# Performance work log

Measured on AMD Instinct MI355X. Metric: run time of the kernel, lower is better.

Reference implementation:

```python
import jax, jax.numpy as jnp
import numpy as np

N_POINTS = 64
N_COLS = 500000
N_ANGS = N_POINTS * (N_POINTS - 1) // 2  # 2016


def setup_inputs() -> dict:
    key = jax.random.key(0)
    k1, k2 = jax.random.split(key)
    X = jax.random.normal(k1, (N_POINTS, N_COLS), dtype=jnp.float32)
    angles = 0.1 * jax.random.normal(k2, (N_ANGS,), dtype=jnp.float32)
    mus = jnp.ones((N_POINTS,), dtype=jnp.float32)
    return {"X": X, "angles": angles, "mus": mus}


def reference(X, angles, mus):
    # X: [n, m]; apply n(n-1)/2 sequential Givens rotations over row pairs
    # in order (iTop, iBtm) for iTop < iBtm, then scale rows by mus.
    # Original torch math per pair: vt' = c*vt - s*vb ; vb' = s*vt + c*vb.
    n = X.shape[0]
    top_np, btm_np = np.triu_indices(n, k=1)  # row-major order matches the double loop
    top = jnp.asarray(top_np, dtype=jnp.int32)
    btm = jnp.asarray(btm_np, dtype=jnp.int32)

    def step(Y, inp):
        a, it, ib = inp
        c = jnp.cos(a)
        s = jnp.sin(a)
        vt = Y[it]  # [m]
        vb = Y[ib]  # [m]
        Y = Y.at[it].set(c * vt - s * vb)
        Y = Y.at[ib].set(s * vt + c * vb)
        return Y, None

    Y, _ = jax.lax.scan(step, X, (angles, top, btm))
    return Y * mus[:, None]
```

## Files before the change

kernel.cpp:

```cpp
#include <hip/hip_runtime.h>
#include <hip/hip_bf16.h>

#define NPTS  64
#define NCOLS 500000
#define NANG  2016

typedef __attribute__((ext_vector_type(8))) short bf16x8;
typedef __attribute__((ext_vector_type(4))) float f32x4;

static __device__ inline short f2bf(float f) {
    union { float f; unsigned u; } uf; uf.f = f;
    unsigned u = uf.u;
    unsigned r = (u + 0x7fffu + ((u >> 16) & 1u)) >> 16;
    return (short)r;
}

__global__ __launch_bounds__(64) void build_M(const float* __restrict__ angles,
                                              const float* __restrict__ mus,
                                              float* __restrict__ Mout) {
    __shared__ float cs[NANG];
    __shared__ float sn[NANG];
    const int tid = threadIdx.x;

    for (int k = tid; k < NANG; k += 64) {
        float a = angles[k];
        cs[k] = cosf(a);
        sn[k] = sinf(a);
    }
    __syncthreads();

    float q[NPTS];
#pragma unroll
    for (int j = 0; j < NPTS; ++j) q[j] = (j == tid) ? 1.0f : 0.0f;

    int k = 0;
#pragma unroll
    for (int i = 0; i < NPTS - 1; ++i) {
#pragma unroll
        for (int ib = i + 1; ib < NPTS; ++ib, ++k) {
            float c = cs[k], s = sn[k];
            float t = q[i];
            float b = q[ib];
            q[ib] = s * t + c * b;
            q[i]  = c * t - s * b;
        }
    }

#pragma unroll
    for (int row = 0; row < NPTS; ++row)
        Mout[row * NPTS + tid] = mus[row] * q[row];
}

__global__ __launch_bounds__(256) void apply_M(const float* __restrict__ X,
                                               const float* __restrict__ M,
                                               float* __restrict__ out,
                                               int nfull, int wstride) {
    const int lane  = threadIdx.x & 63;
    const int wave  = threadIdx.x >> 6;
    const int laneN = lane & 15;
    const int quad  = lane >> 4;

    bf16x8 afrag[4][2];
#pragma unroll
    for (int t = 0; t < 4; ++t) {
#pragma unroll
        for (int q = 0; q < 2; ++q) {
            const float* src = M + (t * 16 + laneN) * NPTS + q * 32 + quad * 8;
            bf16x8 f;
#pragma unroll
            for (int j = 0; j < 8; ++j) f[j] = f2bf(src[j]);
            afrag[t][q] = f;
        }
    }

    const int gw = blockIdx.x * 4 + wave;

    for (int s = gw; s < nfull; s += wstride) {
        const long col0 = (long)s * 64 + 4 * laneN;
        const float* xb = X + col0;

        bf16x8 bfrag[4][2];
#pragma unroll
        for (int q = 0; q < 2; ++q) {
#pragma unroll
            for (int j = 0; j < 8; ++j) {
                const int kk = q * 32 + quad * 8 + j;
                f32x4 v = *(const f32x4*)(xb + (long)kk * NCOLS);
#pragma unroll
                for (int u = 0; u < 4; ++u)
                    bfrag[u][q][j] = f2bf(v[u]);
            }
        }

#pragma unroll
        for (int t = 0; t < 4; ++t) {
            f32x4 acc[4];
#pragma unroll
            for (int u = 0; u < 4; ++u) {
                f32x4 a = {0.f, 0.f, 0.f, 0.f};
                a = __builtin_amdgcn_mfma_f32_16x16x32_bf16(afrag[t][0], bfrag[u][0], a, 0, 0, 0);
                a = __builtin_amdgcn_mfma_f32_16x16x32_bf16(afrag[t][1], bfrag[u][1], a, 0, 0, 0);
                acc[u] = a;
            }
#pragma unroll
            for (int rr = 0; rr < 4; ++rr) {
                const int row = t * 16 + quad * 4 + rr;
                f32x4 o = { acc[0][rr], acc[1][rr], acc[2][rr], acc[3][rr] };
                *(f32x4*)(out + (long)row * NCOLS + col0) = o;
            }
        }
    }

    if (gw < 2) {
        const int col = nfull * 64 + gw * 16 + laneN;
        const float* xb = X + col;
        bf16x8 bfrag[2];
#pragma unroll
        for (int q = 0; q < 2; ++q) {
            bf16x8 f;
#pragma unroll
            for (int j = 0; j < 8; ++j)
                f[j] = f2bf(xb[(long)(q * 32 + quad * 8 + j) * NCOLS]);
            bfrag[q] = f;
        }
#pragma unroll
        for (int t = 0; t < 4; ++t) {
            f32x4 a = {0.f, 0.f, 0.f, 0.f};
            a = __builtin_amdgcn_mfma_f32_16x16x32_bf16(afrag[t][0], bfrag[0], a, 0, 0, 0);
            a = __builtin_amdgcn_mfma_f32_16x16x32_bf16(afrag[t][1], bfrag[1], a, 0, 0, 0);
#pragma unroll
            for (int rr = 0; rr < 4; ++rr)
                out[(long)(t * 16 + quad * 4 + rr) * NCOLS + col] = a[rr];
        }
    }
}

extern "C" void kernel_launch(void* const* d_in, const int* in_sizes, int n_in,
                              void* d_out, int out_size, void* d_ws, size_t ws_size,
                              hipStream_t stream) {
    const float* X      = (const float*)d_in[0];
    const float* angles = (const float*)d_in[1];
    const float* mus    = (const float*)d_in[2];
    float* out = (float*)d_out;
    float* M   = (float*)d_ws;

    build_M<<<1, 64, 0, stream>>>(angles, mus, M);

    const int nfull  = NCOLS / 64;
    const int blocks = 1024;
    apply_M<<<blocks, 256, 0, stream>>>(X, M, out, nfull, blocks * 4);
}
```

Baseline: 322.3 us.

## Parallelize rotation-matrix build into chunk products and combine, use nontemporal stores

The serial single-block build of the 64x64 rotation matrix is split into four blocks, each computing the product of a contiguous chunk of Givens rotations. Two combine launches then multiply the partial products together, applying mus in the last one. The output stores in apply_M become nontemporal, and the grid grows to 1953 blocks so each wave handles about one column tile. The aim is to shorten the serial prologue and improve streaming write behavior, at the cost of two extra small kernel launches.

Measured after the change: 280.6 us. 1.15x faster.

```diff
diff --git a/kernel.cpp b/kernel.cpp
--- a/kernel.cpp
+++ b/kernel.cpp
@@ -15,40 +15,89 @@
     return (short)r;
 }
 
-__global__ __launch_bounds__(64) void build_M(const float* __restrict__ angles,
-                                              const float* __restrict__ mus,
-                                              float* __restrict__ Mout) {
-    __shared__ float cs[NANG];
-    __shared__ float sn[NANG];
+static __host__ __device__ constexpr int rotS(int i) { return 63 * i - i * (i - 1) / 2; }
+
+template<int I0, int I1>
+__device__ __forceinline__ void chunk_body(const float* __restrict__ angles,
+                                           float* __restrict__ P,
+                                           float2* csn) {
+    constexpr int K0 = rotS(I0);
+    constexpr int NK = rotS(I1) - K0;
     const int tid = threadIdx.x;
 
-    for (int k = tid; k < NANG; k += 64) {
-        float a = angles[k];
-        cs[k] = cosf(a);
-        sn[k] = sinf(a);
+    for (int t = tid; t < NK; t += 64) {
+        float s, c;
+        sincosf(angles[K0 + t], &s, &c);
+        csn[t] = make_float2(c, s);
     }
     __syncthreads();
 
-    float q[NPTS];
-#pragma unroll
-    for (int j = 0; j < NPTS; ++j) q[j] = (j == tid) ? 1.0f : 0.0f;
+    float q[64 - I0];
+#pragma unroll
+    for (int r = I0; r < 64; ++r) q[r - I0] = (r == tid) ? 1.0f : 0.0f;
 
     int k = 0;
 #pragma unroll
-    for (int i = 0; i < NPTS - 1; ++i) {
-#pragma unroll
-        for (int ib = i + 1; ib < NPTS; ++ib, ++k) {
-            float c = cs[k], s = sn[k];
-            float t = q[i];
-            float b = q[ib];
-            q[ib] = s * t + c * b;
-            q[i]  = c * t - s * b;
-        }
-    }
-
-#pragma unroll
-    for (int row = 0; row < NPTS; ++row)
-        Mout[row * NPTS + tid] = mus[row] * q[row];
+    for (int i = I0; i < I1; ++i) {
+#pragma unroll
+        for (int ib = i + 1; ib < 64; ++ib, ++k) {
+            float c = csn[k].x, s = csn[k].y;
+            float t = q[i - I0], b = q[ib - I0];
+            q[ib - I0] = s * t + c * b;
+            q[i - I0]  = c * t - s * b;
+        }
+        P[i * 64 + tid] = q[i - I0];
+    }
+#pragma unroll
+    for (int r = 0; r < I0; ++r) P[r * 64 + tid] = (r == tid) ? 1.0f : 0.0f;
+#pragma unroll
+    for (int r = I1; r < 64; ++r) P[r * 64 + tid] = q[r - I0];
+}
+
+__global__ __launch_bounds__(64) void chunk_products(const float* __restrict__ angles,
+                                                     float* __restrict__ ws) {
+    __shared__ float2 csn[531];
+    switch (blockIdx.x) {
+        case 0: chunk_body< 0,  9>(angles, ws + 0 * 4096, csn); break;
+        case 1: chunk_body< 9, 19>(angles, ws + 1 * 4096, csn); break;
+        case 2: chunk_body<19, 32>(angles, ws + 2 * 4096, csn); break;
+        default: chunk_body<32, 63>(angles, ws + 3 * 4096, csn); break;
+    }
+}
+
+__global__ __launch_bounds__(256) void combine(float* __restrict__ ws,
+                                               int lo_off, int hi_off, int out_off,
+                                               int blk_stride,
+                                               const float* __restrict__ mus) {
+    const float* lo = ws + lo_off  + blockIdx.x * blk_stride;
+    const float* hi = ws + hi_off  + blockIdx.x * blk_stride;
+    float*      co  = ws + out_off + blockIdx.x * blk_stride;
+    const int col = threadIdx.x & 63;
+    const int rg  = __builtin_amdgcn_readfirstlane(threadIdx.x >> 6);
+
+    float acc[16] = {0.f};
+#pragma unroll 4
+    for (int k0 = 0; k0 < 64; k0 += 4) {
+        float lo0 = lo[(k0 + 0) * 64 + col];
+        float lo1 = lo[(k0 + 1) * 64 + col];
+        float lo2 = lo[(k0 + 2) * 64 + col];
+        float lo3 = lo[(k0 + 3) * 64 + col];
+#pragma unroll
+        for (int r = 0; r < 16; ++r) {
+            f32x4 h = *(const f32x4*)(hi + (rg * 16 + r) * 64 + k0);
+            acc[r] = fmaf(h[0], lo0, acc[r]);
+            acc[r] = fmaf(h[1], lo1, acc[r]);
+            acc[r] = fmaf(h[2], lo2, acc[r]);
+            acc[r] = fmaf(h[3], lo3, acc[r]);
+        }
+    }
+    __syncthreads();
+#pragma unroll
+    for (int r = 0; r < 16; ++r) {
+        float v = acc[r];
+        if (mus) v *= mus[rg * 16 + r];
+        co[(rg * 16 + r) * 64 + col] = v;
+    }
 }
 
 __global__ __launch_bounds__(256) void apply_M(const float* __restrict__ X,
@@ -106,7 +155,7 @@
             for (int rr = 0; rr < 4; ++rr) {
                 const int row = t * 16 + quad * 4 + rr;
                 f32x4 o = { acc[0][rr], acc[1][rr], acc[2][rr], acc[3][rr] };
-                *(f32x4*)(out + (long)row * NCOLS + col0) = o;
+                __builtin_nontemporal_store(o, (f32x4*)(out + (long)row * NCOLS + col0));
             }
         }
     }
@@ -130,7 +179,8 @@
             a = __builtin_amdgcn_mfma_f32_16x16x32_bf16(afrag[t][1], bfrag[1], a, 0, 0, 0);
 #pragma unroll
             for (int rr = 0; rr < 4; ++rr)
-                out[(long)(t * 16 + quad * 4 + rr) * NCOLS + col] = a[rr];
+                __builtin_nontemporal_store(a[rr],
+                    out + (long)(t * 16 + quad * 4 + rr) * NCOLS + col);
         }
     }
 }
@@ -142,11 +192,13 @@
     const float* angles = (const float*)d_in[1];
     const float* mus    = (const float*)d_in[2];
     float* out = (float*)d_out;
-    float* M   = (float*)d_ws;
-
-    build_M<<<1, 64, 0, stream>>>(angles, mus, M);
+    float* wsf = (float*)d_ws;
+
+    chunk_products<<<4, 64, 0, stream>>>(angles, wsf);
+    combine<<<2, 256, 0, stream>>>(wsf, 0, 4096, 0, 8192, nullptr);
+    combine<<<1, 256, 0, stream>>>(wsf, 0, 2 * 4096, 4096, 0, mus);
 
     const int nfull  = NCOLS / 64;
-    const int blocks = 1024;
-    apply_M<<<blocks, 256, 0, stream>>>(X, M, out, nfull, blocks * 4);
-}
+    const int blocks = 1953;
+    apply_M<<<blocks, 256, 0, stream>>>(X, wsf + 4096, out, nfull, blocks * 4);
+}
```
